# Kernel tuning notes

Measured on AMD Instinct MI355X. Metric: run time of the kernel, lower is better.

The kernel has to match this reference:

```python
import jax, jax.numpy as jnp
from jax import lax
import numpy as np

VGG_C = 512
INNER = 32


def _conv3x3(x, w, b):
    # x: [B,C,H,W], w: [O,I,3,3], padding=1 (SAME)
    y = lax.conv_general_dilated(x, w, (1, 1), 'SAME',
                                 dimension_numbers=('NCHW', 'OIHW', 'NCHW'))
    return y + b[None, :, None, None]


def _predict_filter(style, cw, cb, fw, fb):
    # FilterPredictor_S: conv 512->32, global mean pool, FC 32 -> 9*32*32
    s = _conv3x3(style, cw, cb)                     # [B,32,H,W]
    pooled = s.mean(axis=(2, 3))                    # [B,32]
    f = pooled @ fw.T + fb                          # [B,9216]
    return f.reshape(-1, INNER, INNER, 3, 3)        # [B,outC,inC,3,3]


def _apply_filter(x, filt):
    # per-sample dynamic 3x3 conv: x [B,32,H,W], filt [B,32,32,3,3]
    def one(xi, wi):
        return lax.conv_general_dilated(xi[None], wi, (1, 1), 'SAME',
                                        dimension_numbers=('NCHW', 'OIHW', 'NCHW'))[0]
    return jax.vmap(one)(x, filt)


def setup_inputs() -> dict:
    key = jax.random.key(0)
    ks = jax.random.split(key, 16)
    B, H, W = 8, 64, 64
    sc = 0.02
    d = {
        'content': jax.random.normal(ks[0], (B, VGG_C, H, W), jnp.float32),
        'style': jax.random.normal(ks[1], (B, VGG_C, H, W), jnp.float32),
        'ds_w': jax.random.normal(ks[2], (INNER, VGG_C, 3, 3), jnp.float32) * sc,
        'ds_b': jnp.zeros((INNER,), jnp.float32),
        'up_w': jax.random.normal(ks[3], (VGG_C, INNER, 3, 3), jnp.float32) * sc,
        'up_b': jnp.zeros((VGG_C,), jnp.float32),
        'f1_cw': jax.random.normal(ks[4], (INNER, VGG_C, 3, 3), jnp.float32) * sc,
        'f1_cb': jnp.zeros((INNER,), jnp.float32),
        'f1_fw': jax.random.normal(ks[5], (9 * INNER * INNER, INNER), jnp.float32) * sc,
        'f1_fb': jnp.zeros((9 * INNER * INNER,), jnp.float32),
        'f2_cw': jax.random.normal(ks[6], (INNER, VGG_C, 3, 3), jnp.float32) * sc,
        'f2_cb': jnp.zeros((INNER,), jnp.float32),
        'f2_fw': jax.random.normal(ks[7], (9 * INNER * INNER, INNER), jnp.float32) * sc,
        'f2_fb': jnp.zeros((9 * INNER * INNER,), jnp.float32),
    }
    return d


def reference(content, style, ds_w, ds_b, up_w, up_b,
              f1_cw, f1_cb, f1_fw, f1_fb,
              f2_cw, f2_cb, f2_fw, f2_fb):
    c = _conv3x3(content, ds_w, ds_b)                       # [B,32,H,W]
    filt1 = _predict_filter(style, f1_cw, f1_cb, f1_fw, f1_fb)
    c = _apply_filter(c, filt1)
    c = jnp.where(c >= 0, c, 0.2 * c)                       # LeakyReLU(0.2)
    filt2 = _predict_filter(style, f2_cw, f2_cb, f2_fw, f2_fb)
    c = _apply_filter(c, filt2)
    return content + _conv3x3(c, up_w, up_b)
```

## Files before the change

### kernel.cpp

```cpp
#include <hip/hip_runtime.h>
#include <hip/hip_bf16.h>

#define NB 8
#define NC 512
#define HW 4096
#define INNER 32

typedef unsigned short u16;
typedef unsigned int u32;
typedef __attribute__((ext_vector_type(8))) short bf16x8;
typedef __attribute__((ext_vector_type(4))) float f32x4;

__device__ __forceinline__ float b2f(u16 u) {
    union { u32 a; float f; } z;
    z.a = ((u32)u) << 16;
    return z.f;
}

__device__ __forceinline__ u16 f2b(float v) {
    u32 x = __float_as_uint(v);
    return (u16)((x + 0x7fffu + ((x >> 16) & 1u)) >> 16);
}

__device__ __forceinline__ float ldin(const void* p, int idx, int isf32) {
    if (isf32) return ((const float*)p)[idx];
    return b2f(((const u16*)p)[idx]);
}

__device__ __forceinline__ void gld_lds16(const void* g, void* l) {
    __builtin_amdgcn_global_load_lds(
        (const __attribute__((address_space(1))) unsigned int*)g,
        (__attribute__((address_space(3))) unsigned int*)l, 16, 0, 0);
}

__device__ __forceinline__ int resolve_isf32(int hisf, const void* content) {
    if (hisf >= 0) return hisf;
    int lane = threadIdx.x & 63;
    u16 u = ((const u16*)content)[lane * 2048];
    int e = (u >> 7) & 0xff;
    unsigned long long m = __ballot(e >= 100 && e <= 150);
    return (__popcll(m) < 32) ? 1 : 0;
}


__device__ __forceinline__ void role_style(int bc, const void* style,
        const void* cw1, const void* cw2, float* pooled_raw,
        int isf32, float* smf) {
    int b = bc >> 9, c = bc & 511;
    int base = bc * HW;
    int tid = threadIdx.x;
    float t = 0.f, top = 0.f, bot = 0.f, lft = 0.f, rgt = 0.f;
    if (isf32) {
        const float4* sp = (const float4*)((const float*)style + base);
#pragma unroll
        for (int k = 0; k < 4; k++) {
            int q = tid + k * 256;
            float4 v = sp[q];
            float s4 = (v.x + v.y) + (v.z + v.w);
            int h = q >> 4, w0 = (q & 15) * 4;
            t += s4;
            if (h == 0)   top += s4;
            if (h == 63)  bot += s4;
            if (w0 == 0)  lft += v.x;
            if (w0 == 60) rgt += v.w;
        }
    } else {
        const uint4* sp = (const uint4*)((const u16*)style + base);
#pragma unroll
        for (int k = 0; k < 2; k++) {
            int q = tid + k * 256;
            uint4 v = sp[q];
            float e0 = b2f((u16)(v.x & 0xffffu)), e1 = b2f((u16)(v.x >> 16));
            float e2 = b2f((u16)(v.y & 0xffffu)), e3 = b2f((u16)(v.y >> 16));
            float e4 = b2f((u16)(v.z & 0xffffu)), e5 = b2f((u16)(v.z >> 16));
            float e6 = b2f((u16)(v.w & 0xffffu)), e7 = b2f((u16)(v.w >> 16));
            float s8 = ((e0 + e1) + (e2 + e3)) + ((e4 + e5) + (e6 + e7));
            int h = q >> 3, w0 = (q & 7) * 8;
            t += s8;
            if (h == 0)   top += s8;
            if (h == 63)  bot += s8;
            if (w0 == 0)  lft += e0;
            if (w0 == 56) rgt += e7;
        }
    }
#pragma unroll
    for (int off = 32; off > 0; off >>= 1) {
        t   += __shfl_down(t, off);
        top += __shfl_down(top, off);
        bot += __shfl_down(bot, off);
        lft += __shfl_down(lft, off);
        rgt += __shfl_down(rgt, off);
    }
    int wave = tid >> 6;
    if ((tid & 63) == 0) {
        smf[20 + wave * 5 + 0] = t;   smf[20 + wave * 5 + 1] = top;
        smf[20 + wave * 5 + 2] = bot; smf[20 + wave * 5 + 3] = lft;
        smf[20 + wave * 5 + 4] = rgt;
    }
    __syncthreads();
    if (tid == 0) {
        t   = smf[20] + smf[25] + smf[30] + smf[35];
        top = smf[21] + smf[26] + smf[31] + smf[36];
        bot = smf[22] + smf[27] + smf[32] + smf[37];
        lft = smf[23] + smf[28] + smf[33] + smf[38];
        rgt = smf[24] + smf[29] + smf[34] + smf[39];
        float c00 = ldin(style, base + 0,    isf32);
        float c0W = ldin(style, base + 63,   isf32);
        float cH0 = ldin(style, base + 4032, isf32);
        float cHW = ldin(style, base + 4095, isf32);
        smf[0] = t - bot - rgt + cHW;
        smf[1] = t - bot;
        smf[2] = t - bot - lft + cH0;
        smf[3] = t - rgt;
        smf[4] = t;
        smf[5] = t - lft;
        smf[6] = t - top - rgt + c0W;
        smf[7] = t - top;
        smf[8] = t - top - lft + c00;
    }
    __syncthreads();
    if (tid < 64) {
        int set = tid >> 5, o = tid & 31;
        const void* cw = set ? cw2 : cw1;
        int wb = (o * NC + c) * 9;
        float acc = 0.f;
#pragma unroll
        for (int k = 0; k < 9; k++) acc += ldin(cw, wb + k, isf32) * smf[k];
        atomicAdd(&pooled_raw[(set * NB + b) * 32 + o], acc);
    }
}

__device__ __forceinline__ void role_transform(int ridx, const void* content,
        u16* cT, int bstart, int isf32, float* lds) {
    int hp = ridx & 31;
    int ci = (ridx >> 5) & 15;
    int b4 = ridx >> 9;
    int tid = threadIdx.x;
    size_t gbase = ((size_t)(bstart + b4) * NC + ci * 32) * HW + (size_t)hp * 128;
    if (isf32) {
#pragma unroll
        for (int r2 = 0; r2 < 2; r2++)
#pragma unroll
            for (int k = 0; k < 2; k++) {
                int q = tid + k * 256;
                int c = q >> 4, w0 = (q & 15) * 4;
                float4 v = *(const float4*)((const float*)content
                            + gbase + (size_t)c * HW + r2 * 64 + w0);
                float* dst = lds + r2 * 2080 + c * 65 + w0;
                dst[0] = v.x; dst[1] = v.y; dst[2] = v.z; dst[3] = v.w;
            }
    } else {
#pragma unroll
        for (int r2 = 0; r2 < 2; r2++) {
            int c = tid >> 3, w0 = (tid & 7) * 8;
            uint4 v = *(const uint4*)((const u16*)content
                        + gbase + (size_t)c * HW + r2 * 64 + w0);
            float* dst = lds + r2 * 2080 + c * 65 + w0;
            dst[0] = b2f((u16)(v.x & 0xffffu));
            dst[1] = b2f((u16)(v.x >> 16));
            dst[2] = b2f((u16)(v.y & 0xffffu));
            dst[3] = b2f((u16)(v.y >> 16));
            dst[4] = b2f((u16)(v.z & 0xffffu));
            dst[5] = b2f((u16)(v.z >> 16));
            dst[6] = b2f((u16)(v.w & 0xffffu));
            dst[7] = b2f((u16)(v.w >> 16));
        }
    }
    __syncthreads();
#pragma unroll
    for (int r2 = 0; r2 < 2; r2++) {
        u32* out = (u32*)(cT + ((size_t)(b4 * 16 + ci) * 4096
                                + (hp * 2 + r2) * 64) * 32);
        const float* src = lds + r2 * 2080;
#pragma unroll
        for (int k = 0; k < 4; k++) {
            int j = tid + k * 256;
            int w = j >> 4, cpair = j & 15;
            int key = (w + 1) & 3;
            int p0 = cpair << 1;
            int lc = (((p0 >> 3) ^ key) << 3) | (p0 & 7);
            out[j] = (u32)f2b(src[lc * 65 + w])
                   | ((u32)f2b(src[(lc + 1) * 65 + w]) << 16);
        }
    }
}

__device__ __forceinline__ void role_prep_wdown(int ridx, const void* dsw,
        u16* Bp, int isf32) {
    int idx = ridx * 256 + threadIdx.x;
    int e = idx & 7, l = (idx >> 3) & 63, nf = (idx >> 9) & 1;
    int cb = (idx >> 10) & 15, t9 = idx >> 14;
    int oc = nf * 16 + (l & 15);
    int c = cb * 32 + (l >> 4) * 8 + e;
    Bp[idx] = f2b(ldin(dsw, (oc * NC + c) * 9 + t9, isf32));
}

__device__ __forceinline__ void role_prep_wup(int ridx, const void* upw,
        u16* B2p, int isf32) {
    int idx = ridx * 256 + threadIdx.x;
    int e = idx & 7, l = (idx >> 3) & 63, nfo = (idx >> 9) & 31, t9 = idx >> 14;
    int oc = nfo * 16 + (l & 15);
    int ic = (l >> 4) * 8 + e;
    B2p[idx] = f2b(ldin(upw, (oc * INNER + ic) * 9 + t9, isf32));
}

__device__ __forceinline__ void role_fc(int ridx, const float* pooled_raw,
        const void* cbf1, const void* cbf2,
        const void* fw1, const void* fb1, const void* fw2, const void* fb2,
        u16* fpack, int isf32, float* p) {
    int set = ridx / 288;
    int rr = ridx - set * 288;
    int b = rr / 36;
    int chunk = rr - b * 36;
    int row = chunk * 256 + threadIdx.x;
    const void* fw = set ? fw2 : fw1;
    const void* fb = set ? fb2 : fb1;
    if (threadIdx.x < 32)
        p[threadIdx.x] = pooled_raw[(set * NB + b) * 32 + threadIdx.x]
                           * (1.0f / 4096.0f)
                       + ldin(set ? cbf2 : cbf1, threadIdx.x, isf32);
    __syncthreads();
    float acc = ldin(fb, row, isf32);
    if (isf32) {
        const float* fwf = (const float*)fw + row * 32;
#pragma unroll
        for (int j = 0; j < 32; j++) acc += fwf[j] * p[j];
    } else {
        const u32* w32 = (const u32*)((const u16*)fw + row * 32);
#pragma unroll
        for (int j = 0; j < 16; j++) {
            u32 u = w32[j];
            acc += b2f((u16)(u & 0xffffu)) * p[2 * j];
            acc += b2f((u16)(u >> 16)) * p[2 * j + 1];
        }
    }
    int oc = row / 288;
    int rem = row - oc * 288;
    int ic = rem / 9;
    int t9 = rem - ic * 9;
    int l = (oc & 15) | ((ic >> 3) << 4);
    int e = ic & 7;
    int nf = oc >> 4;
    fpack[((((set * NB + b) * 9 + t9) * 2 + nf) * 64 + l) * 8 + e] = f2b(acc);
}

__device__ __forceinline__ void role_conv_down(int x, const u16* cT,
        const u16* Bp, const void* dsb, u16* c0T, int bstart, int isf32,
        u16* lds) {
    u32* lds32 = (u32*)lds;
    int b4 = x >> 6, row = x & 63;
    int b = bstart + b4;
    int tid = threadIdx.x, lane = tid & 63;
    int wid = __builtin_amdgcn_readfirstlane(tid >> 6);
    for (int i = tid; i < 3 * 66 * 16; i += 256) lds32[i] = 0u;
    __syncthreads();

    int m = lane & 15, g = lane >> 4;
    int wbase = wid * 16;
    f32x4 acc0 = {0.f, 0.f, 0.f, 0.f}, acc1 = {0.f, 0.f, 0.f, 0.f};

    for (int ci = 0; ci < 16; ci++) {
        if (ci) __syncthreads();
        const u16* sp = cT + ((size_t)(b4 * 16 + ci) * 4096) * 32;
#pragma unroll
        for (int r = 0; r < 3; r++) {
            int gh = row + r - 1;
            if (gh >= 0 && gh < 64)
                gld_lds16(sp + (size_t)gh * 2048 + tid * 8,
                          (char*)lds + (r * 66 + 1) * 64 + wid * 1024);
        }
        __syncthreads();
#pragma unroll
        for (int t9 = 0; t9 < 9; t9++) {
            int dh = t9 / 3, dw = t9 - dh * 3;
            int wi = wbase + m + dw;
            bf16x8 a = *(const bf16x8*)(lds + ((dh * 66 + wi) * 32 + ((g ^ (wi & 3)) * 8)));
            bf16x8 b0 = ((const bf16x8*)Bp)[((t9 * 16 + ci) * 2 + 0) * 64 + lane];
            bf16x8 b1 = ((const bf16x8*)Bp)[((t9 * 16 + ci) * 2 + 1) * 64 + lane];
            acc0 = __builtin_amdgcn_mfma_f32_16x16x32_bf16(a, b0, acc0, 0, 0, 0);
            acc1 = __builtin_amdgcn_mfma_f32_16x16x32_bf16(a, b1, acc1, 0, 0, 0);
        }
    }
    float bia0 = ldin(dsb, m, isf32);
    float bia1 = ldin(dsb, 16 + m, isf32);
    size_t obase = ((size_t)b * 4096 + row * 64) * 32;
    int pix0 = wbase + g * 4;
#pragma unroll
    for (int r = 0; r < 4; r++) {
        int w = pix0 + r;
        int key = (w + 1) & 3;
        int p0 = (((m >> 3) ^ key) << 3) | (m & 7);
        int p1 = ((((16 + m) >> 3) ^ key) << 3) | (m & 7);
        c0T[obase + (size_t)w * 32 + p0] = f2b(acc0[r] + bia0);
        c0T[obase + (size_t)w * 32 + p1] = f2b(acc1[r] + bia1);
    }
}


__global__ __launch_bounds__(256) void k_front(
        const void* __restrict__ style,
        const void* __restrict__ cw1, const void* __restrict__ cw2,
        float* __restrict__ pooled_raw, int nStyle,
        const void* __restrict__ content, u16* __restrict__ cT, int bstart, int nT,
        const void* __restrict__ dsw, u16* __restrict__ Bp,
        const void* __restrict__ upw, u16* __restrict__ B2p, int nPrep,
        int hisf) {
    __shared__ float smf[2 * 2080];
    int isf32 = resolve_isf32(hisf, content);
    int x = blockIdx.x;
    if (x < nStyle) { role_style(x, style, cw1, cw2, pooled_raw, isf32, smf); return; }
    x -= nStyle;
    if (x < nT) { role_transform(x, content, cT, bstart, isf32, smf); return; }
    x -= nT;
    if (x < nPrep) { role_prep_wdown(x, dsw, Bp, isf32); return; }
    x -= nPrep;
    role_prep_wup(x, upw, B2p, isf32);
}

__global__ __launch_bounds__(256) void k_mid(
        const u16* __restrict__ cT, const u16* __restrict__ Bp,
        const void* __restrict__ dsb, u16* __restrict__ c0T, int bstart, int nCD,
        const float* __restrict__ pooled_raw,
        const void* __restrict__ cbf1, const void* __restrict__ cbf2,
        const void* __restrict__ fw1, const void* __restrict__ fb1,
        const void* __restrict__ fw2, const void* __restrict__ fb2,
        u16* __restrict__ fpack, const void* __restrict__ content, int hisf) {
    __shared__ u16 lds[3 * 66 * 32];
    int isf32 = resolve_isf32(hisf, content);
    int x = blockIdx.x;
    if (x < nCD) { role_conv_down(x, cT, Bp, dsb, c0T, bstart, isf32, lds); return; }
    role_fc(x - nCD, pooled_raw, cbf1, cbf2, fw1, fb1, fw2, fb2, fpack,
            isf32, (float*)lds);
}

__global__ __launch_bounds__(256) void k_apply(const u16* __restrict__ srcT,
        const u16* __restrict__ fpack, u16* __restrict__ dstT, int lrelu) {
    int b = blockIdx.x >> 6, row = blockIdx.x & 63;
    int tid = threadIdx.x, lane = tid & 63;
    int wid = __builtin_amdgcn_readfirstlane(tid >> 6);
    __shared__ u16 lds[3 * 66 * 32];
    u32* lds32 = (u32*)lds;
    for (int i = tid; i < 96; i += 256) {
        int r = i >> 5, side = (i >> 4) & 1, cpr = i & 15;
        lds32[(r * 66 + side * 65) * 16 + cpr] = 0u;
    }
    const u16* sp = srcT + (size_t)b * 64 * 64 * 32;
    for (int r = 0; r < 3; r++) {
        int gh = row + r - 1;
        u32 ldsoff = (u32)(r * 66 + 1) * 64 + (u32)wid * 1024;
        if (gh >= 0 && gh < 64) {
            gld_lds16(sp + (size_t)gh * 2048 + tid * 8, (char*)lds + ldsoff);
        } else {
            int4 z = make_int4(0, 0, 0, 0);
            *(int4*)((char*)lds + ldsoff + (u32)lane * 16) = z;
        }
    }
    __syncthreads();

    int m = lane & 15, g = lane >> 4, wbase = wid * 16;
    f32x4 acc0 = {0.f, 0.f, 0.f, 0.f}, acc1 = {0.f, 0.f, 0.f, 0.f};
    const bf16x8* FB = (const bf16x8*)fpack + (size_t)b * 1152;
#pragma unroll
    for (int t9 = 0; t9 < 9; t9++) {
        int dh = t9 / 3, dw = t9 - dh * 3;
        int wi = wbase + m + dw;
        bf16x8 a = *(const bf16x8*)(lds + ((dh * 66 + wi) * 32 + ((g ^ (wi & 3)) * 8)));
        bf16x8 b0 = FB[(t9 * 2 + 0) * 64 + lane];
        bf16x8 b1 = FB[(t9 * 2 + 1) * 64 + lane];
        acc0 = __builtin_amdgcn_mfma_f32_16x16x32_bf16(a, b0, acc0, 0, 0, 0);
        acc1 = __builtin_amdgcn_mfma_f32_16x16x32_bf16(a, b1, acc1, 0, 0, 0);
    }
    size_t obase = ((size_t)(b * 64 + row) * 64) * 32;
    int pix0 = wbase + g * 4;
#pragma unroll
    for (int r = 0; r < 4; r++) {
        float v0 = acc0[r], v1 = acc1[r];
        if (lrelu) {
            v0 = (v0 >= 0.f) ? v0 : 0.2f * v0;
            v1 = (v1 >= 0.f) ? v1 : 0.2f * v1;
        }
        int w = pix0 + r;
        int key = (w + 1) & 3;
        int p0 = (((m >> 3) ^ key) << 3) | (m & 7);
        int p1 = ((((16 + m) >> 3) ^ key) << 3) | (m & 7);
        dstT[obase + (size_t)w * 32 + p0] = f2b(v0);
        dstT[obase + (size_t)w * 32 + p1] = f2b(v1);
    }
}

__global__ __launch_bounds__(256) void k_conv_up(const u16* __restrict__ c2T,
        const u16* __restrict__ B2p, const void* __restrict__ upb,
        const void* __restrict__ content, void* __restrict__ outv, int hisf) {
    int isf32 = resolve_isf32(hisf, content);
    int b = blockIdx.x >> 6, row = blockIdx.x & 63;
    int nq = blockIdx.y;
    int tid = threadIdx.x, lane = tid & 63;
    int wid = __builtin_amdgcn_readfirstlane(tid >> 6);
    __shared__ char smem[64 * 68 * 4] __attribute__((aligned(16)));
    u16* lds = (u16*)smem;
    u32* lds32 = (u32*)smem;
    for (int i = tid; i < 96; i += 256) {
        int r = i >> 5, side = (i >> 4) & 1, cpr = i & 15;
        lds32[(r * 66 + side * 65) * 16 + cpr] = 0u;
    }
    const u16* sp = c2T + (size_t)b * 64 * 64 * 32;
    for (int r = 0; r < 3; r++) {
        int gh = row + r - 1;
        u32 ldsoff = (u32)(r * 66 + 1) * 64 + (u32)wid * 1024;
        if (gh >= 0 && gh < 64) {
            gld_lds16(sp + (size_t)gh * 2048 + tid * 8, (char*)lds + ldsoff);
        } else {
            int4 z = make_int4(0, 0, 0, 0);
            *(int4*)((char*)lds + ldsoff + (u32)lane * 16) = z;
        }
    }
    __syncthreads();

    int m = lane & 15, g = lane >> 4, wbase = wid * 16;
    f32x4 acc[8];
#pragma unroll
    for (int i = 0; i < 8; i++) acc[i] = (f32x4){0.f, 0.f, 0.f, 0.f};
#pragma unroll
    for (int t9 = 0; t9 < 9; t9++) {
        int dh = t9 / 3, dw = t9 - dh * 3;
        int wi = wbase + m + dw;
        bf16x8 a = *(const bf16x8*)(lds + ((dh * 66 + wi) * 32 + ((g ^ (wi & 3)) * 8)));
#pragma unroll
        for (int nfl = 0; nfl < 8; nfl++) {
            bf16x8 bw = ((const bf16x8*)B2p)[(t9 * 32 + nq * 8 + nfl) * 64 + lane];
            acc[nfl] = __builtin_amdgcn_mfma_f32_16x16x32_bf16(a, bw, acc[nfl], 0, 0, 0);
        }
    }

    int pix0 = wbase + g * 4;
    float* fl = (float*)smem;
    int ocl2 = tid >> 4;
    int px0 = (tid & 15) * 4;
    __syncthreads();
#pragma unroll
    for (int hf = 0; hf < 2; hf++) {
        if (hf) __syncthreads();
#pragma unroll
        for (int nf = 0; nf < 4; nf++) {
            int ocl = nf * 16 + m;
            *(f32x4*)(fl + ocl * 68 + pix0) = acc[hf * 4 + nf];
        }
        __syncthreads();
#pragma unroll
        for (int p = 0; p < 4; p++) {
            int ocl = p * 16 + ocl2;
            int oc = nq * 128 + hf * 64 + ocl;
            float bias = ldin(upb, oc, isf32);
            f32x4 v4 = *(const f32x4*)(fl + ocl * 68 + px0);
            size_t idx = ((size_t)b * NC + oc) * HW + (size_t)row * 64 + px0;
            if (isf32) {
                f32x4 rsd = *(const f32x4*)((const float*)content + idx);
                f32x4 ov;
#pragma unroll
                for (int r = 0; r < 4; r++) ov[r] = v4[r] + bias + rsd[r];
                *(f32x4*)((float*)outv + idx) = ov;
            } else {
                ushort4 rv = *(const ushort4*)((const u16*)content + idx);
                ushort4 ov;
                ov.x = f2b(v4[0] + bias + b2f(rv.x));
                ov.y = f2b(v4[1] + bias + b2f(rv.y));
                ov.z = f2b(v4[2] + bias + b2f(rv.z));
                ov.w = f2b(v4[3] + bias + b2f(rv.w));
                *(ushort4*)((u16*)outv + idx) = ov;
            }
        }
    }
}

extern "C" void kernel_launch(void* const* d_in, const int* in_sizes, int n_in,
                              void* d_out, int out_size, void* d_ws, size_t ws_size,
                              hipStream_t stream) {
    const void* content = d_in[0];
    const void* style   = d_in[1];
    const void* ds_w    = d_in[2];
    const void* ds_b    = d_in[3];
    const void* up_w    = d_in[4];
    const void* up_b    = d_in[5];
    const void* f1_cw   = d_in[6];
    const void* f1_cb   = d_in[7];
    const void* f1_fw   = d_in[8];
    const void* f1_fb   = d_in[9];
    const void* f2_cw   = d_in[10];
    const void* f2_cb   = d_in[11];
    const void* f2_fw   = d_in[12];
    const void* f2_fb   = d_in[13];

    int hisf = -1;
    if (in_sizes && n_in >= 1) {
        if (in_sizes[0] == NB * NC * HW * 4) hisf = 1;
        else if (in_sizes[0] == NB * NC * HW * 2) hisf = 0;
    }

    const size_t SZ_PACK = 294912;
    const size_t SZ_CT2  = 2097152;
    const size_t REQ_WS  = 3 * SZ_CT2 + 3 * SZ_PACK + 2048 + 64;

    if (ws_size >= REQ_WS) {
        char* w = (char*)d_ws;
        u16*   B2pack = (u16*)w;                 w += SZ_PACK;
        u16*   c2T    = (u16*)w;                 w += SZ_CT2;
        u16*   c0T    = (u16*)w;                 w += SZ_CT2;
        u16*   c1T    = (u16*)w;                 w += SZ_CT2;
        u16*   Bpack  = (u16*)w;                 w += SZ_PACK;
        u16*   fpack  = (u16*)w;                 w += SZ_PACK;
        float* pooled_raw = (float*)w;
        u16*   cT     = (u16*)d_out;

        hipMemsetAsync(pooled_raw, 0, 2 * NB * 32 * 4, stream);
        k_front<<<4096 + 4096 + 2 * 576, 256, 0, stream>>>(
            style, f1_cw, f2_cw, pooled_raw, 4096,
            content, cT, 0, 4096,
            ds_w, Bpack, up_w, B2pack, 576, hisf);
        k_mid<<<512 + 576, 256, 0, stream>>>(
            cT, Bpack, ds_b, c0T, 0, 512,
            pooled_raw, f1_cb, f2_cb,
            f1_fw, f1_fb, f2_fw, f2_fb, fpack, content, hisf);
        k_apply<<<NB * 64, 256, 0, stream>>>(c0T, fpack, c1T, 1);
        k_apply<<<NB * 64, 256, 0, stream>>>(c1T, fpack + NB * 9216, c2T, 0);
        k_conv_up<<<dim3(NB * 64, 4), 256, 0, stream>>>(c2T, B2pack, up_b,
                                                        content, d_out, hisf);
    } else {
        float* pooled_raw = (float*)d_out;
        u16*   fpack  = (u16*)(pooled_raw + 512);
        u16*   Bpack  = fpack + 147456;
        u16*   c0T    = Bpack + 147456;
        u16*   c1T    = c0T + 1048576;
        u16*   cTh    = c1T + 1048576;
        u16*   B2pack = (u16*)d_ws;
        u16*   c2T    = B2pack + 147456;

        hipMemsetAsync(pooled_raw, 0, 2 * NB * 32 * 4, stream);
        k_front<<<4096 + 2048 + 2 * 576, 256, 0, stream>>>(
            style, f1_cw, f2_cw, pooled_raw, 4096,
            content, cTh, 0, 2048,
            ds_w, Bpack, up_w, B2pack, 576, hisf);
        k_mid<<<256 + 576, 256, 0, stream>>>(
            cTh, Bpack, ds_b, c0T, 0, 256,
            pooled_raw, f1_cb, f2_cb,
            f1_fw, f1_fb, f2_fw, f2_fb, fpack, content, hisf);
        k_front<<<2048, 256, 0, stream>>>(
            style, f1_cw, f2_cw, pooled_raw, 0,
            content, cTh, 4, 2048,
            ds_w, Bpack, up_w, B2pack, 0, hisf);
        k_mid<<<256, 256, 0, stream>>>(
            cTh, Bpack, ds_b, c0T, 4, 256,
            pooled_raw, f1_cb, f2_cb,
            f1_fw, f1_fb, f2_fw, f2_fb, fpack, content, hisf);
        k_apply<<<NB * 64, 256, 0, stream>>>(c0T, fpack, c1T, 1);
        k_apply<<<NB * 64, 256, 0, stream>>>(c1T, fpack + NB * 9216, c2T, 0);
        k_conv_up<<<dim3(NB * 64, 4), 256, 0, stream>>>(c2T, B2pack, up_b,
                                                        content, d_out, hisf);
    }
}
```

Baseline: 283.7 us.

## Fuse the two dynamic filter applications into one kernel with halo recompute

Merges the two per-sample dynamic 3x3 conv passes into a single kernel. Each block loads five input rows and computes three rows of the first filtered output, with LeakyReLU, into LDS. It then applies the second filter from LDS, removing the c1T intermediate round trip and one launch. The down-conv and FC roles move to 512-thread blocks with one output-channel fragment per wave, and conv_up now prefetches the residual content before the epilogue. The cost is recomputing the halo rows of the first pass and using more LDS per block.

```diff
diff --git a/kernel.cpp b/kernel.cpp
--- a/kernel.cpp
+++ b/kernel.cpp
@@ -208,11 +208,11 @@
         const void* cbf1, const void* cbf2,
         const void* fw1, const void* fb1, const void* fw2, const void* fb2,
         u16* fpack, int isf32, float* p) {
-    int set = ridx / 288;
-    int rr = ridx - set * 288;
-    int b = rr / 36;
-    int chunk = rr - b * 36;
-    int row = chunk * 256 + threadIdx.x;
+    int set = ridx / 144;
+    int rr = ridx - set * 144;
+    int b = rr / 18;
+    int chunk = rr - b * 18;
+    int row = chunk * 512 + threadIdx.x;
     const void* fw = set ? fw2 : fw1;
     const void* fb = set ? fb2 : fb1;
     if (threadIdx.x < 32)
@@ -252,22 +252,23 @@
     int b = bstart + b4;
     int tid = threadIdx.x, lane = tid & 63;
     int wid = __builtin_amdgcn_readfirstlane(tid >> 6);
-    for (int i = tid; i < 3 * 66 * 16; i += 256) lds32[i] = 0u;
+    for (int i = tid; i < 3 * 66 * 16; i += 512) lds32[i] = 0u;
     __syncthreads();
 
     int m = lane & 15, g = lane >> 4;
-    int wbase = wid * 16;
-    f32x4 acc0 = {0.f, 0.f, 0.f, 0.f}, acc1 = {0.f, 0.f, 0.f, 0.f};
+    int wq = wid & 3, ocf = wid >> 2;
+    int wbase = wq * 16;
+    int sr = wid >> 1, sh = wid & 1;
+    f32x4 acc = {0.f, 0.f, 0.f, 0.f};
 
     for (int ci = 0; ci < 16; ci++) {
         if (ci) __syncthreads();
         const u16* sp = cT + ((size_t)(b4 * 16 + ci) * 4096) * 32;
-#pragma unroll
-        for (int r = 0; r < 3; r++) {
-            int gh = row + r - 1;
+        if (wid < 6) {
+            int gh = row + sr - 1;
             if (gh >= 0 && gh < 64)
-                gld_lds16(sp + (size_t)gh * 2048 + tid * 8,
-                          (char*)lds + (r * 66 + 1) * 64 + wid * 1024);
+                gld_lds16(sp + (size_t)gh * 2048 + (sh * 64 + lane) * 8,
+                          (char*)lds + (sr * 66 + 1) * 64 + sh * 1024);
         }
         __syncthreads();
 #pragma unroll
@@ -275,24 +276,20 @@
             int dh = t9 / 3, dw = t9 - dh * 3;
             int wi = wbase + m + dw;
             bf16x8 a = *(const bf16x8*)(lds + ((dh * 66 + wi) * 32 + ((g ^ (wi & 3)) * 8)));
-            bf16x8 b0 = ((const bf16x8*)Bp)[((t9 * 16 + ci) * 2 + 0) * 64 + lane];
-            bf16x8 b1 = ((const bf16x8*)Bp)[((t9 * 16 + ci) * 2 + 1) * 64 + lane];
-            acc0 = __builtin_amdgcn_mfma_f32_16x16x32_bf16(a, b0, acc0, 0, 0, 0);
-            acc1 = __builtin_amdgcn_mfma_f32_16x16x32_bf16(a, b1, acc1, 0, 0, 0);
-        }
-    }
-    float bia0 = ldin(dsb, m, isf32);
-    float bia1 = ldin(dsb, 16 + m, isf32);
+            bf16x8 bb = ((const bf16x8*)Bp)[((t9 * 16 + ci) * 2 + ocf) * 64 + lane];
+            acc = __builtin_amdgcn_mfma_f32_16x16x32_bf16(a, bb, acc, 0, 0, 0);
+        }
+    }
+    int oc = ocf * 16 + m;
+    float bia = ldin(dsb, oc, isf32);
     size_t obase = ((size_t)b * 4096 + row * 64) * 32;
     int pix0 = wbase + g * 4;
 #pragma unroll
     for (int r = 0; r < 4; r++) {
         int w = pix0 + r;
         int key = (w + 1) & 3;
-        int p0 = (((m >> 3) ^ key) << 3) | (m & 7);
-        int p1 = ((((16 + m) >> 3) ^ key) << 3) | (m & 7);
-        c0T[obase + (size_t)w * 32 + p0] = f2b(acc0[r] + bia0);
-        c0T[obase + (size_t)w * 32 + p1] = f2b(acc1[r] + bia1);
+        int p = (((oc >> 3) ^ key) << 3) | (oc & 7);
+        c0T[obase + (size_t)w * 32 + p] = f2b(acc[r] + bia);
     }
 }
 
@@ -317,7 +314,7 @@
     role_prep_wup(x, upw, B2p, isf32);
 }
 
-__global__ __launch_bounds__(256) void k_mid(
+__global__ __launch_bounds__(512) void k_mid(
         const u16* __restrict__ cT, const u16* __restrict__ Bp,
         const void* __restrict__ dsb, u16* __restrict__ c0T, int bstart, int nCD,
         const float* __restrict__ pooled_raw,
@@ -333,58 +330,88 @@
             isf32, (float*)lds);
 }
 
-__global__ __launch_bounds__(256) void k_apply(const u16* __restrict__ srcT,
-        const u16* __restrict__ fpack, u16* __restrict__ dstT, int lrelu) {
+__global__ __launch_bounds__(512) void k_apply2(const u16* __restrict__ c0T,
+        const u16* __restrict__ fpack, u16* __restrict__ c2T) {
     int b = blockIdx.x >> 6, row = blockIdx.x & 63;
     int tid = threadIdx.x, lane = tid & 63;
     int wid = __builtin_amdgcn_readfirstlane(tid >> 6);
-    __shared__ u16 lds[3 * 66 * 32];
-    u32* lds32 = (u32*)lds;
-    for (int i = tid; i < 96; i += 256) {
-        int r = i >> 5, side = (i >> 4) & 1, cpr = i & 15;
-        lds32[(r * 66 + side * 65) * 16 + cpr] = 0u;
-    }
-    const u16* sp = srcT + (size_t)b * 64 * 64 * 32;
-    for (int r = 0; r < 3; r++) {
-        int gh = row + r - 1;
-        u32 ldsoff = (u32)(r * 66 + 1) * 64 + (u32)wid * 1024;
-        if (gh >= 0 && gh < 64) {
-            gld_lds16(sp + (size_t)gh * 2048 + tid * 8, (char*)lds + ldsoff);
-        } else {
-            int4 z = make_int4(0, 0, 0, 0);
-            *(int4*)((char*)lds + ldsoff + (u32)lane * 16) = z;
-        }
-    }
-    __syncthreads();
-
-    int m = lane & 15, g = lane >> 4, wbase = wid * 16;
-    f32x4 acc0 = {0.f, 0.f, 0.f, 0.f}, acc1 = {0.f, 0.f, 0.f, 0.f};
-    const bf16x8* FB = (const bf16x8*)fpack + (size_t)b * 1152;
+    __shared__ u16 A[5 * 66 * 32];
+    __shared__ u16 B[3 * 66 * 32];
+    u32* A32 = (u32*)A;
+    u32* B32 = (u32*)B;
+    for (int i = tid; i < 160; i += 512) {
+        int r = i / 32, side = (i >> 4) & 1, cpr = i & 15;
+        A32[(r * 66 + side * 65) * 16 + cpr] = 0u;
+    }
+    for (int i = tid; i < 3 * 66 * 16; i += 512) B32[i] = 0u;
+    const u16* sp = c0T + (size_t)b * 4096 * 32;
+#pragma unroll
+    for (int i = 0; i < 3; i++) {
+        int t = wid + i * 8;
+        if (t < 20) {
+            int r = t >> 2, seg = t & 3;
+            int gh = row + r - 2;
+            char* dst = (char*)A + r * 4224 + 64 + seg * 1024;
+            if (gh >= 0 && gh < 64) {
+                gld_lds16(sp + (size_t)gh * 2048 + (seg * 64 + lane) * 8, dst);
+            } else {
+                *(int4*)(dst + (u32)lane * 16) = make_int4(0, 0, 0, 0);
+            }
+        }
+    }
+    __syncthreads();
+
+    int m = lane & 15, g = lane >> 4;
+    int wq = wid & 3, ocf = wid >> 2;
+    int wbase = wq * 16;
+    int oc = ocf * 16 + m;
+    const bf16x8* FB1 = (const bf16x8*)fpack + (size_t)b * 1152;
+    const bf16x8* FB2 = (const bf16x8*)fpack + (size_t)(NB + b) * 1152;
+
+#pragma unroll
+    for (int rr = 0; rr < 3; rr++) {
+        int gh1 = row - 1 + rr;
+        f32x4 acc = {0.f, 0.f, 0.f, 0.f};
+#pragma unroll
+        for (int t9 = 0; t9 < 9; t9++) {
+            int dh = t9 / 3, dw = t9 - dh * 3;
+            int wi = wbase + m + dw;
+            bf16x8 a = *(const bf16x8*)(A + ((rr + dh) * 66 + wi) * 32
+                                          + ((g ^ (wi & 3)) * 8));
+            bf16x8 bb = FB1[(t9 * 2 + ocf) * 64 + lane];
+            acc = __builtin_amdgcn_mfma_f32_16x16x32_bf16(a, bb, acc, 0, 0, 0);
+        }
+        if (gh1 >= 0 && gh1 < 64) {
+#pragma unroll
+            for (int r = 0; r < 4; r++) {
+                float v = acc[r];
+                v = (v >= 0.f) ? v : 0.2f * v;
+                int w = wbase + g * 4 + r;
+                int wi2 = w + 1;
+                int p = (((oc >> 3) ^ (wi2 & 3)) << 3) | (oc & 7);
+                B[(rr * 66 + wi2) * 32 + p] = f2b(v);
+            }
+        }
+    }
+    __syncthreads();
+
+    f32x4 acc = {0.f, 0.f, 0.f, 0.f};
 #pragma unroll
     for (int t9 = 0; t9 < 9; t9++) {
         int dh = t9 / 3, dw = t9 - dh * 3;
         int wi = wbase + m + dw;
-        bf16x8 a = *(const bf16x8*)(lds + ((dh * 66 + wi) * 32 + ((g ^ (wi & 3)) * 8)));
-        bf16x8 b0 = FB[(t9 * 2 + 0) * 64 + lane];
-        bf16x8 b1 = FB[(t9 * 2 + 1) * 64 + lane];
-        acc0 = __builtin_amdgcn_mfma_f32_16x16x32_bf16(a, b0, acc0, 0, 0, 0);
-        acc1 = __builtin_amdgcn_mfma_f32_16x16x32_bf16(a, b1, acc1, 0, 0, 0);
+        bf16x8 a = *(const bf16x8*)(B + (dh * 66 + wi) * 32
+                                      + ((g ^ (wi & 3)) * 8));
+        bf16x8 bb = FB2[(t9 * 2 + ocf) * 64 + lane];
+        acc = __builtin_amdgcn_mfma_f32_16x16x32_bf16(a, bb, acc, 0, 0, 0);
     }
     size_t obase = ((size_t)(b * 64 + row) * 64) * 32;
-    int pix0 = wbase + g * 4;
 #pragma unroll
     for (int r = 0; r < 4; r++) {
-        float v0 = acc0[r], v1 = acc1[r];
-        if (lrelu) {
-            v0 = (v0 >= 0.f) ? v0 : 0.2f * v0;
-            v1 = (v1 >= 0.f) ? v1 : 0.2f * v1;
-        }
-        int w = pix0 + r;
+        int w = wbase + g * 4 + r;
         int key = (w + 1) & 3;
-        int p0 = (((m >> 3) ^ key) << 3) | (m & 7);
-        int p1 = ((((16 + m) >> 3) ^ key) << 3) | (m & 7);
-        dstT[obase + (size_t)w * 32 + p0] = f2b(v0);
-        dstT[obase + (size_t)w * 32 + p1] = f2b(v1);
+        int p = (((oc >> 3) ^ key) << 3) | (oc & 7);
+        c2T[obase + (size_t)w * 32 + p] = f2b(acc[r]);
     }
 }
 
@@ -437,30 +464,60 @@
     int ocl2 = tid >> 4;
     int px0 = (tid & 15) * 4;
     __syncthreads();
-#pragma unroll
-    for (int hf = 0; hf < 2; hf++) {
-        if (hf) __syncthreads();
-#pragma unroll
-        for (int nf = 0; nf < 4; nf++) {
-            int ocl = nf * 16 + m;
-            *(f32x4*)(fl + ocl * 68 + pix0) = acc[hf * 4 + nf];
-        }
-        __syncthreads();
-#pragma unroll
-        for (int p = 0; p < 4; p++) {
-            int ocl = p * 16 + ocl2;
-            int oc = nq * 128 + hf * 64 + ocl;
-            float bias = ldin(upb, oc, isf32);
-            f32x4 v4 = *(const f32x4*)(fl + ocl * 68 + px0);
-            size_t idx = ((size_t)b * NC + oc) * HW + (size_t)row * 64 + px0;
-            if (isf32) {
-                f32x4 rsd = *(const f32x4*)((const float*)content + idx);
+
+    if (isf32) {
+        f32x4 rsd[2][4];
+#pragma unroll
+        for (int hf = 0; hf < 2; hf++)
+#pragma unroll
+            for (int p = 0; p < 4; p++) {
+                int oc = nq * 128 + hf * 64 + p * 16 + ocl2;
+                rsd[hf][p] = *(const f32x4*)((const float*)content
+                    + ((size_t)b * NC + oc) * HW + (size_t)row * 64 + px0);
+            }
+#pragma unroll
+        for (int hf = 0; hf < 2; hf++) {
+            if (hf) __syncthreads();
+#pragma unroll
+            for (int nf = 0; nf < 4; nf++)
+                *(f32x4*)(fl + (nf * 16 + m) * 68 + pix0) = acc[hf * 4 + nf];
+            __syncthreads();
+#pragma unroll
+            for (int p = 0; p < 4; p++) {
+                int oc = nq * 128 + hf * 64 + p * 16 + ocl2;
+                float bias = ((const float*)upb)[oc];
+                f32x4 v4 = *(const f32x4*)(fl + (p * 16 + ocl2) * 68 + px0);
+                size_t idx = ((size_t)b * NC + oc) * HW + (size_t)row * 64 + px0;
                 f32x4 ov;
 #pragma unroll
-                for (int r = 0; r < 4; r++) ov[r] = v4[r] + bias + rsd[r];
+                for (int r = 0; r < 4; r++) ov[r] = v4[r] + bias + rsd[hf][p][r];
                 *(f32x4*)((float*)outv + idx) = ov;
-            } else {
-                ushort4 rv = *(const ushort4*)((const u16*)content + idx);
+            }
+        }
+    } else {
+        ushort4 rsd[2][4];
+#pragma unroll
+        for (int hf = 0; hf < 2; hf++)
+#pragma unroll
+            for (int p = 0; p < 4; p++) {
+                int oc = nq * 128 + hf * 64 + p * 16 + ocl2;
+                rsd[hf][p] = *(const ushort4*)((const u16*)content
+                    + ((size_t)b * NC + oc) * HW + (size_t)row * 64 + px0);
+            }
+#pragma unroll
+        for (int hf = 0; hf < 2; hf++) {
+            if (hf) __syncthreads();
+#pragma unroll
+            for (int nf = 0; nf < 4; nf++)
+                *(f32x4*)(fl + (nf * 16 + m) * 68 + pix0) = acc[hf * 4 + nf];
+            __syncthreads();
+#pragma unroll
+            for (int p = 0; p < 4; p++) {
+                int oc = nq * 128 + hf * 64 + p * 16 + ocl2;
+                float bias = b2f(((const u16*)upb)[oc]);
+                f32x4 v4 = *(const f32x4*)(fl + (p * 16 + ocl2) * 68 + px0);
+                size_t idx = ((size_t)b * NC + oc) * HW + (size_t)row * 64 + px0;
+                ushort4 rv = rsd[hf][p];
                 ushort4 ov;
                 ov.x = f2b(v4[0] + bias + b2f(rv.x));
                 ov.y = f2b(v4[1] + bias + b2f(rv.y));
@@ -498,14 +555,13 @@
 
     const size_t SZ_PACK = 294912;
     const size_t SZ_CT2  = 2097152;
-    const size_t REQ_WS  = 3 * SZ_CT2 + 3 * SZ_PACK + 2048 + 64;
+    const size_t REQ_WS  = 2 * SZ_CT2 + 3 * SZ_PACK + 2048 + 64;
 
     if (ws_size >= REQ_WS) {
         char* w = (char*)d_ws;
         u16*   B2pack = (u16*)w;                 w += SZ_PACK;
         u16*   c2T    = (u16*)w;                 w += SZ_CT2;
         u16*   c0T    = (u16*)w;                 w += SZ_CT2;
-        u16*   c1T    = (u16*)w;                 w += SZ_CT2;
         u16*   Bpack  = (u16*)w;                 w += SZ_PACK;
         u16*   fpack  = (u16*)w;                 w += SZ_PACK;
         float* pooled_raw = (float*)w;
@@ -516,12 +572,11 @@
             style, f1_cw, f2_cw, pooled_raw, 4096,
             content, cT, 0, 4096,
             ds_w, Bpack, up_w, B2pack, 576, hisf);
-        k_mid<<<512 + 576, 256, 0, stream>>>(
+        k_mid<<<512 + 288, 512, 0, stream>>>(
             cT, Bpack, ds_b, c0T, 0, 512,
             pooled_raw, f1_cb, f2_cb,
             f1_fw, f1_fb, f2_fw, f2_fb, fpack, content, hisf);
-        k_apply<<<NB * 64, 256, 0, stream>>>(c0T, fpack, c1T, 1);
-        k_apply<<<NB * 64, 256, 0, stream>>>(c1T, fpack + NB * 9216, c2T, 0);
+        k_apply2<<<NB * 64, 512, 0, stream>>>(c0T, fpack, c2T);
         k_conv_up<<<dim3(NB * 64, 4), 256, 0, stream>>>(c2T, B2pack, up_b,
                                                         content, d_out, hisf);
     } else {
@@ -529,8 +584,7 @@
         u16*   fpack  = (u16*)(pooled_raw + 512);
         u16*   Bpack  = fpack + 147456;
         u16*   c0T    = Bpack + 147456;
-        u16*   c1T    = c0T + 1048576;
-        u16*   cTh    = c1T + 1048576;
+        u16*   cTh    = c0T + 1048576;
         u16*   B2pack = (u16*)d_ws;
         u16*   c2T    = B2pack + 147456;
 
@@ -539,7 +593,7 @@
             style, f1_cw, f2_cw, pooled_raw, 4096,
             content, cTh, 0, 2048,
             ds_w, Bpack, up_w, B2pack, 576, hisf);
-        k_mid<<<256 + 576, 256, 0, stream>>>(
+        k_mid<<<256 + 288, 512, 0, stream>>>(
             cTh, Bpack, ds_b, c0T, 0, 256,
             pooled_raw, f1_cb, f2_cb,
             f1_fw, f1_fb, f2_fw, f2_fb, fpack, content, hisf);
@@ -547,12 +601,11 @@
             style, f1_cw, f2_cw, pooled_raw, 0,
             content, cTh, 4, 2048,
             ds_w, Bpack, up_w, B2pack, 0, hisf);
-        k_mid<<<256, 256, 0, stream>>>(
+        k_mid<<<256, 512, 0, stream>>>(
             cTh, Bpack, ds_b, c0T, 4, 256,
             pooled_raw, f1_cb, f2_cb,
             f1_fw, f1_fb, f2_fw, f2_fb, fpack, content, hisf);
-        k_apply<<<NB * 64, 256, 0, stream>>>(c0T, fpack, c1T, 1);
-        k_apply<<<NB * 64, 256, 0, stream>>>(c1T, fpack + NB * 9216, c2T, 0);
+        k_apply2<<<NB * 64, 512, 0, stream>>>(c0T, fpack, c2T);
         k_conv_up<<<dim3(NB * 64, 4), 256, 0, stream>>>(c2T, B2pack, up_b,
                                                         content, d_out, hisf);
     }
```

Measured after the change: 280.9 us. No clear change (-1.0%).
